# Kernel tuning notes

Hardware: AMD Instinct MI355X
Metric: run time of the kernel (lower is better)

Reference implementation:

```python
import jax, jax.numpy as jnp
import numpy as np

EPS = 1e-5
NEG_INF = -1e30


def layer_norm_seq(x, gamma, beta):
    # Faithful to the custom LayerNorm: normalizes over dim=1 (the T axis of
    # [B, T, C]) with UNBIASED variance (torch.var default), then scales by
    # gamma/beta of shape [C] broadcast over the last axis.
    m = jnp.mean(x, axis=1, keepdims=True)
    v = jnp.var(x, axis=1, keepdims=True, ddof=1)
    return gamma * (x - m) / jnp.sqrt(v + EPS) + beta


def setup_inputs() -> dict:
    key = jax.random.key(0)
    B, T, C, H = 4, 1024, 1024, 16
    hd = C // H  # 64
    ks = jax.random.split(key, 10)
    s_in = 1.0 / np.sqrt(C)
    s_ff = 1.0 / np.sqrt(4 * C)
    return {
        "x": jax.random.normal(ks[0], (B, T, C), dtype=jnp.float32),
        # NOTE: Head uses self.key(x) for BOTH q and k; the query Linear is
        # dead code, so only key/value weights are materialized.
        "Wk": jax.random.uniform(ks[1], (H, C, hd), minval=-s_in, maxval=s_in, dtype=jnp.float32),
        "Wv": jax.random.uniform(ks[2], (H, C, hd), minval=-s_in, maxval=s_in, dtype=jnp.float32),
        "Wp": jax.random.uniform(ks[3], (C, C), minval=-s_in, maxval=s_in, dtype=jnp.float32),
        "bp": jnp.zeros((C,), dtype=jnp.float32),
        "W1": jax.random.uniform(ks[4], (4 * C, C), minval=-s_in, maxval=s_in, dtype=jnp.float32),
        "b1": jnp.zeros((4 * C,), dtype=jnp.float32),
        "W2": jax.random.uniform(ks[5], (C, 4 * C), minval=-s_ff, maxval=s_ff, dtype=jnp.float32),
        "b2": jnp.zeros((C,), dtype=jnp.float32),
        "g1": jnp.ones((C,), dtype=jnp.float32),
        "beta1": jnp.zeros((C,), dtype=jnp.float32),
        "g2": jnp.ones((C,), dtype=jnp.float32),
        "beta2": jnp.zeros((C,), dtype=jnp.float32),
    }


def reference(x, Wk, Wv, Wp, bp, W1, b1, W2, b2, g1, beta1, g2, beta2):
    B, T, C = x.shape
    H, _, hd = Wk.shape
    scale = hd ** -0.5

    # --- self-attention sublayer (pre-LN over sequence axis) ---
    h = layer_norm_seq(x, g1, beta1)
    # q and k BOTH use the key projection (faithful to the original bug).
    qk = jnp.einsum("btc,hcd->bhtd", h, Wk)          # [B,H,T,hd]
    v = jnp.einsum("btc,hcd->bhtd", h, Wv)           # [B,H,T,hd]
    wei = jnp.einsum("bhtd,bhsd->bhts", qk, qk) * scale  # [B,H,T,T]
    causal = jnp.tril(jnp.ones((T, T), dtype=bool))
    wei = jnp.where(causal, wei, NEG_INF)
    wei = jax.nn.softmax(wei, axis=-1)
    attn = jnp.einsum("bhts,bhsd->bthd", wei, v).reshape(B, T, C)
    attn = attn @ Wp.T + bp
    x = x + attn

    # --- feed-forward sublayer ---
    h2 = layer_norm_seq(x, g2, beta2)
    ff = jax.nn.relu(h2 @ W1.T + b1) @ W2.T + b2
    return x + ff
```

## Files before the change

### kernel.cpp

```cpp
#include <hip/hip_runtime.h>
#include <stdint.h>


#define BDIM 256

typedef __attribute__((ext_vector_type(8))) __bf16 bf16x8;
typedef __attribute__((ext_vector_type(4))) float f32x4;

__device__ __forceinline__ unsigned short f2bf(float f) {
    unsigned u = __float_as_uint(f);
    u += 0x7fff + ((u >> 16) & 1);
    return (unsigned short)(u >> 16);
}

__device__ __forceinline__ void gload_lds16(const void* g, void* l) {
    __builtin_amdgcn_global_load_lds(
        (const __attribute__((address_space(1))) void*)g,
        (__attribute__((address_space(3))) void*)l, 16, 0, 0);
}

__global__ void k_cast_bf16(const float* __restrict__ in, unsigned short* __restrict__ out, int n4) {
    int i = blockIdx.x * BDIM + threadIdx.x;
    if (i >= n4) return;
    float4 v = ((const float4*)in)[i];
    ushort4 o;
    o.x = f2bf(v.x); o.y = f2bf(v.y); o.z = f2bf(v.z); o.w = f2bf(v.w);
    ((ushort4*)out)[i] = o;
}

__global__ void k_headT(const float* __restrict__ W, unsigned short* __restrict__ out) {
    __shared__ float tile[64][65];
    const int tid = threadIdx.x;
    const int c0 = blockIdx.x * 64, h = blockIdx.y;
    const float* src = W + ((long)h << 16) + (long)c0 * 64;
    #pragma unroll
    for (int j = 0; j < 16; ++j) {
        int idx = j * 256 + tid;
        tile[idx >> 6][idx & 63] = src[idx];
    }
    __syncthreads();
    #pragma unroll
    for (int j = 0; j < 16; ++j) {
        int idx = j * 256 + tid;
        int d = idx >> 6, c = idx & 63;
        out[(long)(h * 64 + d) * 1024 + c0 + c] = f2bf(tile[c][d]);
    }
}

__global__ void k_ln_part(const float* __restrict__ x, float* __restrict__ psum, float* __restrict__ psq) {
    int c = blockIdx.x * BDIM + threadIdx.x;
    int tc = blockIdx.y, b = blockIdx.z;
    const float* p = x + ((long)b << 20) + ((long)tc * 128) * 1024 + c;
    float s = 0.f, ss = 0.f;
    for (int t = 0; t < 128; ++t) {
        float v = p[t * 1024];
        s += v; ss += v * v;
    }
    int o = (b * 8 + tc) * 1024 + c;
    psum[o] = s; psq[o] = ss;
}

__global__ void k_ln_fin(const float* __restrict__ psum, const float* __restrict__ psq,
                         float* __restrict__ mean, float* __restrict__ rstd) {
    int i = blockIdx.x * BDIM + threadIdx.x;
    int b = i >> 10, c = i & 1023;
    float s = 0.f, ss = 0.f;
    for (int j = 0; j < 8; ++j) {
        s  += psum[(b * 8 + j) * 1024 + c];
        ss += psq[(b * 8 + j) * 1024 + c];
    }
    float m = s * (1.0f / 1024.0f);
    float var = (ss - 1024.0f * m * m) * (1.0f / 1023.0f);
    mean[i] = m;
    rstd[i] = rsqrtf(var + 1e-5f);
}

__global__ void k_ln_apply(const float* __restrict__ x, const float* __restrict__ mean,
                           const float* __restrict__ rstd, const float* __restrict__ g,
                           const float* __restrict__ beta, unsigned short* __restrict__ out) {
    int i = blockIdx.x * BDIM + threadIdx.x;
    int flat = i << 2;
    int b = flat >> 20, c = flat & 1023;
    float4 xv = ((const float4*)x)[i];
    float4 mv = *(const float4*)&mean[(b << 10) + c];
    float4 rv = *(const float4*)&rstd[(b << 10) + c];
    float4 gv = *(const float4*)&g[c];
    float4 bv = *(const float4*)&beta[c];
    ushort4 o;
    o.x = f2bf(gv.x * (xv.x - mv.x) * rv.x + bv.x);
    o.y = f2bf(gv.y * (xv.y - mv.y) * rv.y + bv.y);
    o.z = f2bf(gv.z * (xv.z - mv.z) * rv.z + bv.z);
    o.w = f2bf(gv.w * (xv.w - mv.w) * rv.w + bv.w);
    ((ushort4*)out)[i] = o;
}

__global__ void k_addbias(const float* __restrict__ res, const float* __restrict__ bias,
                          float* __restrict__ out) {
    int i = blockIdx.x * BDIM + threadIdx.x;
    int c = (i << 2) & 1023;
    float4 r = ((const float4*)res)[i];
    float4 bv = *(const float4*)&bias[c];
    r.x += bv.x; r.y += bv.y; r.z += bv.z; r.w += bv.w;
    ((float4*)out)[i] = r;
}

template <int EPI>
__global__ __launch_bounds__(256, 3) void k_gemm_bt(
    const unsigned short* __restrict__ A, const unsigned short* __restrict__ B,
    void* __restrict__ Cv, const float* __restrict__ bias, const float* __restrict__ res,
    int N, int K, int ldA, int ldB, long sA, long sB, long sC)
{
    __shared__ __align__(16) unsigned short As[2][128 * 32];
    __shared__ __align__(16) unsigned short Bs[2][128 * 32];
    const int tid = threadIdx.x;
    const int wave = tid >> 6, lane = tid & 63;
    const long bz = blockIdx.z;
    const int m0 = blockIdx.y * 128, n0 = blockIdx.x * 128;
    const unsigned short* Ab = A + bz * sA;
    const unsigned short* Bb = B + bz * sB;

    const int srow = wave * 16 + (lane >> 2);
    const int skel = (lane & 3) * 8;
    const unsigned short* gA0 = Ab + (long)(m0 + srow) * ldA + skel;
    const unsigned short* gB0 = Bb + (long)(n0 + srow) * ldB + skel;
    const long rowoffA = (long)64 * ldA;
    const long rowoffB = (long)64 * ldB;
    const int lofs = wave * 512;

    f32x4 acc[4][4] = {};

    const int wm = (wave >> 1) * 64, wn = (wave & 1) * 64;
    const int lr = lane & 15, lg = lane >> 4;
    const int aoff = lg * 8;

    gload_lds16(gA0, &As[0][lofs]);
    gload_lds16(gA0 + rowoffA, &As[0][2048 + lofs]);
    gload_lds16(gB0, &Bs[0][lofs]);
    gload_lds16(gB0 + rowoffB, &Bs[0][2048 + lofs]);
    asm volatile("s_waitcnt vmcnt(0)" ::: "memory");
    __builtin_amdgcn_s_barrier();
    __builtin_amdgcn_sched_barrier(0);

    int cur = 0;
    for (int kt = 0; kt < K; kt += 32) {
        const int nxt = cur ^ 1;
        if (kt + 32 < K) {
            gload_lds16(gA0 + kt + 32, &As[nxt][lofs]);
            gload_lds16(gA0 + rowoffA + kt + 32, &As[nxt][2048 + lofs]);
            gload_lds16(gB0 + kt + 32, &Bs[nxt][lofs]);
            gload_lds16(gB0 + rowoffB + kt + 32, &Bs[nxt][2048 + lofs]);
        }
        bf16x8 af[4], bfr[4];
        #pragma unroll
        for (int i = 0; i < 4; ++i) {
            af[i]  = *(const bf16x8*)&As[cur][(wm + i * 16 + lr) * 32 + aoff];
            bfr[i] = *(const bf16x8*)&Bs[cur][(wn + i * 16 + lr) * 32 + aoff];
        }
        #pragma unroll
        for (int i = 0; i < 4; ++i)
            #pragma unroll
            for (int j = 0; j < 4; ++j)
                acc[i][j] = __builtin_amdgcn_mfma_f32_16x16x32_bf16(af[i], bfr[j], acc[i][j], 0, 0, 0);
        asm volatile("s_waitcnt vmcnt(0)" ::: "memory");
        __builtin_amdgcn_s_barrier();
        __builtin_amdgcn_sched_barrier(0);
        cur = nxt;
    }

    const int cr0 = lg * 4;
    #pragma unroll
    for (int mi = 0; mi < 4; ++mi) {
        #pragma unroll
        for (int r = 0; r < 4; ++r) {
            const int row = m0 + wm + mi * 16 + cr0 + r;
            const long rb = bz * sC + (long)row * N;
            #pragma unroll
            for (int nj = 0; nj < 4; ++nj) {
                const int col = n0 + wn + nj * 16 + lr;
                float v = acc[mi][nj][r];
                if (EPI == 0) {
                    ((unsigned short*)Cv)[rb + col] = f2bf(v);
                } else if (EPI == 1) {
                    ((float*)Cv)[rb + col] = v + bias[col] + res[rb + col];
                } else if (EPI == 2) {
                    v += bias[col];
                    ((unsigned short*)Cv)[rb + col] = f2bf(v > 0.f ? v : 0.f);
                } else {
                    atomicAdd(&((float*)Cv)[rb + col], v);
                }
            }
        }
    }
}

#define CEXP 0.18033688f
#define PSTRIDE 72

__global__ __launch_bounds__(256, 2) void k_attn(
    const unsigned short* __restrict__ qk, const unsigned short* __restrict__ vt,
    unsigned short* __restrict__ ctx)
{
    __shared__ __align__(16) unsigned short Ks[64 * 64];
    __shared__ __align__(16) unsigned short Vs[64 * 64];
    __shared__ __align__(16) unsigned short P[4][16 * PSTRIDE];
    const int tid = threadIdx.x;
    const int wave = tid >> 6, lane = tid & 63;
    const int bh = blockIdx.x >> 3, pairIdx = blockIdx.x & 7;
    const int b = bh >> 4, h = bh & 15;
    const int lr = lane & 15, lg = lane >> 4;

    const int swz = (lr & 7) << 4;
    const int cby0 = (lg * 16) ^ swz;
    const int cby1 = (64 + lg * 16) ^ swz;
    const int srow_l = lane >> 3;
    const int scol = ((lane & 7) * 8) ^ (srow_l << 3);

    unsigned short* Pw = P[wave];
    char* KsB = (char*)Ks;
    char* VsB = (char*)Vs;
    const unsigned short* qbase = qk + ((long)b << 20) + h * 64;
    const unsigned short* vb    = vt + ((long)(b * 16 + h) << 16);

    #pragma unroll 1
    for (int phase = 0; phase < 2; ++phase) {
        const int qb = phase ? (15 - pairIdx) : pairIdx;
        const int q0 = qb << 6;
        const int qw = q0 + wave * 16;

        const unsigned short* qrow = qbase + (long)(qw + lr) * 1024 + lg * 8;
        const bf16x8 aq0 = *(const bf16x8*)qrow;
        const bf16x8 aq1 = *(const bf16x8*)(qrow + 32);

        f32x4 acc[4] = {};
        float mrow[4] = {-1e30f, -1e30f, -1e30f, -1e30f};
        float lrow[4] = {0.f, 0.f, 0.f, 0.f};

        for (int c = 0; c <= qb; ++c) {
            const int k0 = c << 6;
            __syncthreads();
            #pragma unroll
            for (int i = 0; i < 2; ++i) {
                const int row = i * 32 + wave * 8 + srow_l;
                gload_lds16(qbase + (long)(k0 + row) * 1024 + scol,
                            KsB + i * 4096 + wave * 1024);
                gload_lds16(vb + (long)row * 1024 + k0 + scol,
                            VsB + i * 4096 + wave * 1024);
            }
            __syncthreads();

            f32x4 s[4];
            #pragma unroll
            for (int t = 0; t < 4; ++t) {
                const int r = t * 16 + lr;
                bf16x8 bk0 = *(const bf16x8*)(KsB + r * 128 + cby0);
                bf16x8 bk1 = *(const bf16x8*)(KsB + r * 128 + cby1);
                f32x4 z = {};
                z = __builtin_amdgcn_mfma_f32_16x16x32_bf16(aq0, bk0, z, 0, 0, 0);
                s[t] = __builtin_amdgcn_mfma_f32_16x16x32_bf16(aq1, bk1, z, 0, 0, 0);
            }
            if (c == qb) {
                #pragma unroll
                for (int t = 0; t < 4; ++t) {
                    const int col = t * 16 + lr;
                    #pragma unroll
                    for (int r = 0; r < 4; ++r)
                        if (col > wave * 16 + lg * 4 + r) s[t][r] = -1e30f;
                }
            }
            float fac[4];
            #pragma unroll
            for (int r = 0; r < 4; ++r) {
                float v = fmaxf(fmaxf(s[0][r], s[1][r]), fmaxf(s[2][r], s[3][r]));
                v = fmaxf(v, __shfl_xor(v, 1));
                v = fmaxf(v, __shfl_xor(v, 2));
                v = fmaxf(v, __shfl_xor(v, 4));
                v = fmaxf(v, __shfl_xor(v, 8));
                float mn = fmaxf(mrow[r], v);
                fac[r] = exp2f((mrow[r] - mn) * CEXP);
                mrow[r] = mn;
            }
            float psum[4] = {0.f, 0.f, 0.f, 0.f};
            #pragma unroll
            for (int t = 0; t < 4; ++t) {
                #pragma unroll
                for (int r = 0; r < 4; ++r) {
                    float p = exp2f((s[t][r] - mrow[r]) * CEXP);
                    psum[r] += p;
                    Pw[(lg * 4 + r) * PSTRIDE + t * 16 + lr] = f2bf(p);
                }
            }
            #pragma unroll
            for (int r = 0; r < 4; ++r) {
                float v = psum[r];
                v += __shfl_xor(v, 1); v += __shfl_xor(v, 2);
                v += __shfl_xor(v, 4); v += __shfl_xor(v, 8);
                lrow[r] = lrow[r] * fac[r] + v;
            }
            #pragma unroll
            for (int ni = 0; ni < 4; ++ni)
                #pragma unroll
                for (int r = 0; r < 4; ++r)
                    acc[ni][r] *= fac[r];
            const bf16x8 pa0 = *(const bf16x8*)&Pw[lr * PSTRIDE + lg * 8];
            const bf16x8 pa1 = *(const bf16x8*)&Pw[lr * PSTRIDE + 32 + lg * 8];
            #pragma unroll
            for (int ni = 0; ni < 4; ++ni) {
                const int vr = ni * 16 + lr;
                bf16x8 bv0 = *(const bf16x8*)(VsB + vr * 128 + cby0);
                bf16x8 bv1 = *(const bf16x8*)(VsB + vr * 128 + cby1);
                acc[ni] = __builtin_amdgcn_mfma_f32_16x16x32_bf16(pa0, bv0, acc[ni], 0, 0, 0);
                acc[ni] = __builtin_amdgcn_mfma_f32_16x16x32_bf16(pa1, bv1, acc[ni], 0, 0, 0);
            }
        }

        unsigned short* crow = ctx + ((long)(b * 1024 + qw)) * 1024 + h * 64;
        #pragma unroll
        for (int r = 0; r < 4; ++r) {
            const float inv = 1.0f / lrow[r];
            #pragma unroll
            for (int ni = 0; ni < 4; ++ni)
                crow[(long)(lg * 4 + r) * 1024 + ni * 16 + lr] = f2bf(acc[ni][r] * inv);
        }
    }
}

extern "C" void kernel_launch(void* const* d_in, const int* in_sizes, int n_in,
                              void* d_out, int out_size, void* d_ws, size_t ws_size,
                              hipStream_t stream)
{
    const float* x   = (const float*)d_in[0];
    const float* Wk  = (const float*)d_in[1];
    const float* Wv  = (const float*)d_in[2];
    const float* Wp  = (const float*)d_in[3];
    const float* bp  = (const float*)d_in[4];
    const float* W1  = (const float*)d_in[5];
    const float* b1  = (const float*)d_in[6];
    const float* W2  = (const float*)d_in[7];
    const float* b2  = (const float*)d_in[8];
    const float* g1  = (const float*)d_in[9];
    const float* be1 = (const float*)d_in[10];
    const float* g2  = (const float*)d_in[11];
    const float* be2 = (const float*)d_in[12];
    float* out = (float*)d_out;

    char* ws = (char*)d_ws;
    const long MB = 1024 * 1024;
    unsigned short* BkT = (unsigned short*)(ws);
    unsigned short* WvT = (unsigned short*)(ws + 2 * MB);
    unsigned short* WpB = (unsigned short*)(ws + 4 * MB);
    unsigned short* W1B = (unsigned short*)(ws + 6 * MB);
    unsigned short* W2B = (unsigned short*)(ws + 14 * MB);
    unsigned short* hB  = (unsigned short*)(ws + 22 * MB);
    unsigned short* qkB = (unsigned short*)(ws + 30 * MB);
    unsigned short* VtB = (unsigned short*)(ws + 38 * MB);
    unsigned short* ctx = (unsigned short*)(ws + 46 * MB);
    unsigned short* ff1 = (unsigned short*)(ws + 30 * MB);
    float* x2   = (float*)(ws + 62 * MB);
    float* psum = (float*)(ws + 78 * MB);
    float* psq  = (float*)(ws + 78 * MB + 128 * 1024);
    float* mean = (float*)(ws + 78 * MB + 256 * 1024);
    float* rstd = (float*)(ws + 78 * MB + 272 * 1024);

    k_cast_bf16<<<1024, BDIM, 0, stream>>>(Wp, WpB, 262144);
    k_cast_bf16<<<4096, BDIM, 0, stream>>>(W1, W1B, 1048576);
    k_cast_bf16<<<4096, BDIM, 0, stream>>>(W2, W2B, 1048576);
    k_headT<<<dim3(16, 16), BDIM, 0, stream>>>(Wk, BkT);
    k_headT<<<dim3(16, 16), BDIM, 0, stream>>>(Wv, WvT);

    k_ln_part<<<dim3(4, 8, 4), BDIM, 0, stream>>>(x, psum, psq);
    k_ln_fin<<<16, BDIM, 0, stream>>>(psum, psq, mean, rstd);
    k_ln_apply<<<4096, BDIM, 0, stream>>>(x, mean, rstd, g1, be1, hB);

    k_gemm_bt<0><<<dim3(8, 32, 1), BDIM, 0, stream>>>(hB, BkT, qkB, nullptr, nullptr, 1024, 1024, 1024, 1024, 0, 0, 0);
    k_gemm_bt<0><<<dim3(8, 8, 4), BDIM, 0, stream>>>(WvT, hB, VtB, nullptr, nullptr, 1024, 1024, 1024, 1024, 0, MB, MB);

    k_attn<<<512, BDIM, 0, stream>>>(qkB, VtB, ctx);

    k_gemm_bt<1><<<dim3(8, 32, 1), BDIM, 0, stream>>>(ctx, WpB, x2, bp, x, 1024, 1024, 1024, 1024, 0, 0, 0);

    k_ln_part<<<dim3(4, 8, 4), BDIM, 0, stream>>>(x2, psum, psq);
    k_ln_fin<<<16, BDIM, 0, stream>>>(psum, psq, mean, rstd);
    k_ln_apply<<<4096, BDIM, 0, stream>>>(x2, mean, rstd, g2, be2, hB);

    k_gemm_bt<2><<<dim3(32, 32, 1), BDIM, 0, stream>>>(hB, W1B, ff1, b1, nullptr, 4096, 1024, 1024, 1024, 0, 0, 0);

    k_addbias<<<4096, BDIM, 0, stream>>>(x2, b2, out);
    k_gemm_bt<3><<<dim3(8, 32, 2), BDIM, 0, stream>>>(ff1, W2B, out, nullptr, nullptr, 1024, 2048, 4096, 4096, 2048, 2048, 0);
}
```

Baseline: 384.1 us.

## Triple-buffer GEMM LDS pipeline with XOR swizzle and deeper split-K for FF2

Moves the bf16 GEMM from a double-buffered to a triple-buffered LDS pipeline. Tiles are prefetched two steps ahead and the loop waits with vmcnt(4), so one in-flight stage overlaps compute and there is only one barrier per iteration. It also XOR-swizzles the k-chunk position per row on both the global-to-LDS writes and the fragment reads, to reduce LDS bank conflicts. The FF2 GEMM's split-K goes from 2 to 4 slices to raise the block count, at the cost of more atomic or partial-sum traffic into the output and 50% more LDS per block, which may lower occupancy.

```diff
diff --git a/kernel.cpp b/kernel.cpp
--- a/kernel.cpp
+++ b/kernel.cpp
@@ -110,45 +110,53 @@
     void* __restrict__ Cv, const float* __restrict__ bias, const float* __restrict__ res,
     int N, int K, int ldA, int ldB, long sA, long sB, long sC)
 {
-    __shared__ __align__(16) unsigned short As[2][128 * 32];
-    __shared__ __align__(16) unsigned short Bs[2][128 * 32];
+    __shared__ __align__(16) unsigned short As[3][128 * 32];
+    __shared__ __align__(16) unsigned short Bs[3][128 * 32];
     const int tid = threadIdx.x;
     const int wave = tid >> 6, lane = tid & 63;
     const long bz = blockIdx.z;
     const int m0 = blockIdx.y * 128, n0 = blockIdx.x * 128;
-    const unsigned short* Ab = A + bz * sA;
-    const unsigned short* Bb = B + bz * sB;
 
     const int srow = wave * 16 + (lane >> 2);
-    const int skel = (lane & 3) * 8;
-    const unsigned short* gA0 = Ab + (long)(m0 + srow) * ldA + skel;
-    const unsigned short* gB0 = Bb + (long)(n0 + srow) * ldB + skel;
+    const int kbs = (lane & 3) ^ ((srow >> 1) & 3);
+    const unsigned short* gA0 = A + bz * sA + (long)(m0 + srow) * ldA + kbs * 8;
+    const unsigned short* gB0 = B + bz * sB + (long)(n0 + srow) * ldB + kbs * 8;
     const long rowoffA = (long)64 * ldA;
     const long rowoffB = (long)64 * ldB;
     const int lofs = wave * 512;
 
     f32x4 acc[4][4] = {};
-
     const int wm = (wave >> 1) * 64, wn = (wave & 1) * 64;
     const int lr = lane & 15, lg = lane >> 4;
-    const int aoff = lg * 8;
-
-    gload_lds16(gA0, &As[0][lofs]);
-    gload_lds16(gA0 + rowoffA, &As[0][2048 + lofs]);
-    gload_lds16(gB0, &Bs[0][lofs]);
-    gload_lds16(gB0 + rowoffB, &Bs[0][2048 + lofs]);
-    asm volatile("s_waitcnt vmcnt(0)" ::: "memory");
-    __builtin_amdgcn_s_barrier();
-    __builtin_amdgcn_sched_barrier(0);
+    const int aoff = (lg ^ ((lr >> 1) & 3)) * 8;
+
+    const int nsteps = K >> 5;
+
+    auto stage = [&](int step, int buf) {
+        const long ko = (long)step * 32;
+        unsigned short* a = &As[buf][lofs];
+        unsigned short* b = &Bs[buf][lofs];
+        gload_lds16(gA0 + ko, a);
+        gload_lds16(gA0 + rowoffA + ko, a + 2048);
+        gload_lds16(gB0 + ko, b);
+        gload_lds16(gB0 + rowoffB + ko, b + 2048);
+    };
+
+    stage(0, 0);
+    stage(1, 1);
 
     int cur = 0;
-    for (int kt = 0; kt < K; kt += 32) {
-        const int nxt = cur ^ 1;
-        if (kt + 32 < K) {
-            gload_lds16(gA0 + kt + 32, &As[nxt][lofs]);
-            gload_lds16(gA0 + rowoffA + kt + 32, &As[nxt][2048 + lofs]);
-            gload_lds16(gB0 + kt + 32, &Bs[nxt][lofs]);
-            gload_lds16(gB0 + rowoffB + kt + 32, &Bs[nxt][2048 + lofs]);
+    for (int t = 0; t < nsteps; ++t) {
+        if (t + 1 < nsteps) {
+            asm volatile("s_waitcnt vmcnt(4)" ::: "memory");
+        } else {
+            asm volatile("s_waitcnt vmcnt(0)" ::: "memory");
+        }
+        __builtin_amdgcn_s_barrier();
+        __builtin_amdgcn_sched_barrier(0);
+        if (t + 2 < nsteps) {
+            int pbuf = cur + 2; if (pbuf >= 3) pbuf -= 3;
+            stage(t + 2, pbuf);
         }
         bf16x8 af[4], bfr[4];
         #pragma unroll
@@ -161,10 +169,8 @@
             #pragma unroll
             for (int j = 0; j < 4; ++j)
                 acc[i][j] = __builtin_amdgcn_mfma_f32_16x16x32_bf16(af[i], bfr[j], acc[i][j], 0, 0, 0);
-        asm volatile("s_waitcnt vmcnt(0)" ::: "memory");
-        __builtin_amdgcn_s_barrier();
         __builtin_amdgcn_sched_barrier(0);
-        cur = nxt;
+        cur = cur + 1; if (cur == 3) cur = 0;
     }
 
     const int cr0 = lg * 4;
@@ -385,5 +391,5 @@
     k_gemm_bt<2><<<dim3(32, 32, 1), BDIM, 0, stream>>>(hB, W1B, ff1, b1, nullptr, 4096, 1024, 1024, 1024, 0, 0, 0);
 
     k_addbias<<<4096, BDIM, 0, stream>>>(x2, b2, out);
-    k_gemm_bt<3><<<dim3(8, 32, 2), BDIM, 0, stream>>>(ff1, W2B, out, nullptr, nullptr, 1024, 2048, 4096, 4096, 2048, 2048, 0);
-}
+    k_gemm_bt<3><<<dim3(8, 32, 4), BDIM, 0, stream>>>(ff1, W2B, out, nullptr, nullptr, 1024, 1024, 4096, 4096, 1024, 1024, 0);
+}
```

Result: slower. 420.3 us (+9.4%).

## Add 256x256 tiled GEMM for FFN and XOR-swizzle LDS layout

Applied to the files above, without the earlier changes.

Adds a new 512-thread GEMM kernel with 256x256 output tiles and a K-step of 64, used for both FFN GEMMs (the second one now split-K over four slices with atomic adds). The LDS tiles in both this kernel and the existing 128x128 GEMM are XOR-swizzled on the k-chunk index to cut LDS bank conflicts on fragment reads. The larger tile raises arithmetic intensity per load and adds setprio around the MFMA bursts. In exchange it uses more registers and LDS per block, launches fewer blocks (256 for FFN1), and the deeper split-K adds more atomic traffic into the output.

```diff
diff --git a/kernel.cpp b/kernel.cpp
--- a/kernel.cpp
+++ b/kernel.cpp
@@ -116,27 +116,28 @@
     const int wave = tid >> 6, lane = tid & 63;
     const long bz = blockIdx.z;
     const int m0 = blockIdx.y * 128, n0 = blockIdx.x * 128;
-    const unsigned short* Ab = A + bz * sA;
-    const unsigned short* Bb = B + bz * sB;
 
     const int srow = wave * 16 + (lane >> 2);
-    const int skel = (lane & 3) * 8;
-    const unsigned short* gA0 = Ab + (long)(m0 + srow) * ldA + skel;
-    const unsigned short* gB0 = Bb + (long)(n0 + srow) * ldB + skel;
+    const int kbs = (lane & 3) ^ ((srow >> 1) & 3);
+    const unsigned short* gA0 = A + bz * sA + (long)(m0 + srow) * ldA + kbs * 8;
+    const unsigned short* gB0 = B + bz * sB + (long)(n0 + srow) * ldB + kbs * 8;
     const long rowoffA = (long)64 * ldA;
     const long rowoffB = (long)64 * ldB;
     const int lofs = wave * 512;
 
     f32x4 acc[4][4] = {};
-
     const int wm = (wave >> 1) * 64, wn = (wave & 1) * 64;
     const int lr = lane & 15, lg = lane >> 4;
-    const int aoff = lg * 8;
-
-    gload_lds16(gA0, &As[0][lofs]);
-    gload_lds16(gA0 + rowoffA, &As[0][2048 + lofs]);
-    gload_lds16(gB0, &Bs[0][lofs]);
-    gload_lds16(gB0 + rowoffB, &Bs[0][2048 + lofs]);
+    const int aoff = (lg ^ ((lr >> 1) & 3)) * 8;
+
+    auto stage = [&](int kt, int buf) {
+        gload_lds16(gA0 + kt, &As[buf][lofs]);
+        gload_lds16(gA0 + rowoffA + kt, &As[buf][2048 + lofs]);
+        gload_lds16(gB0 + kt, &Bs[buf][lofs]);
+        gload_lds16(gB0 + rowoffB + kt, &Bs[buf][2048 + lofs]);
+    };
+
+    stage(0, 0);
     asm volatile("s_waitcnt vmcnt(0)" ::: "memory");
     __builtin_amdgcn_s_barrier();
     __builtin_amdgcn_sched_barrier(0);
@@ -144,12 +145,7 @@
     int cur = 0;
     for (int kt = 0; kt < K; kt += 32) {
         const int nxt = cur ^ 1;
-        if (kt + 32 < K) {
-            gload_lds16(gA0 + kt + 32, &As[nxt][lofs]);
-            gload_lds16(gA0 + rowoffA + kt + 32, &As[nxt][2048 + lofs]);
-            gload_lds16(gB0 + kt + 32, &Bs[nxt][lofs]);
-            gload_lds16(gB0 + rowoffB + kt + 32, &Bs[nxt][2048 + lofs]);
-        }
+        if (kt + 32 < K) stage(kt + 32, nxt);
         bf16x8 af[4], bfr[4];
         #pragma unroll
         for (int i = 0; i < 4; ++i) {
@@ -182,7 +178,102 @@
                     ((unsigned short*)Cv)[rb + col] = f2bf(v);
                 } else if (EPI == 1) {
                     ((float*)Cv)[rb + col] = v + bias[col] + res[rb + col];
-                } else if (EPI == 2) {
+                } else {
+                    v += bias[col];
+                    ((unsigned short*)Cv)[rb + col] = f2bf(v > 0.f ? v : 0.f);
+                }
+            }
+        }
+    }
+}
+
+template <int EPI>
+__global__ __launch_bounds__(512, 2) void k_gemm256(
+    const unsigned short* __restrict__ A, const unsigned short* __restrict__ B,
+    void* __restrict__ Cv, const float* __restrict__ bias,
+    int N, int K, int ldA, int ldB)
+{
+    __shared__ __align__(16) unsigned short As[2][2][128 * 64];
+    __shared__ __align__(16) unsigned short Bs[2][2][128 * 64];
+    const int tid = threadIdx.x;
+    const int wv = tid >> 6, l = tid & 63;
+    const int m0 = blockIdx.y * 256, n0 = blockIdx.x * 256;
+    const long koff = (long)blockIdx.z * K;
+
+    const int lr = l & 15, lg = l >> 4;
+
+    const int srow = wv * 16 + (l >> 3);
+    const int g0 = (l & 7) ^ (l >> 4);
+    const int g1 = (l & 7) ^ (4 + (l >> 4));
+    const unsigned short* pA = A + koff + (long)(m0 + srow) * ldA;
+    const unsigned short* pB = B + koff + (long)(n0 + srow) * ldB;
+    const long l8A = (long)8 * ldA, l128A = (long)128 * ldA;
+    const long l8B = (long)8 * ldB, l128B = (long)128 * ldB;
+    const int dst0 = wv * 1024;
+
+    auto stage = [&](int k0, int d) {
+        #pragma unroll
+        for (int h = 0; h < 2; ++h) {
+            gload_lds16(pA + (long)h * l128A + k0 + g0 * 8, &As[d][h][dst0]);
+            gload_lds16(pA + (long)h * l128A + l8A + k0 + g1 * 8, &As[d][h][dst0 + 512]);
+            gload_lds16(pB + (long)h * l128B + k0 + g0 * 8, &Bs[d][h][dst0]);
+            gload_lds16(pB + (long)h * l128B + l8B + k0 + g1 * 8, &Bs[d][h][dst0 + 512]);
+        }
+    };
+
+    f32x4 acc[8][4] = {};
+    const int wh = wv >> 2;
+    const int bh = (wv & 3) >> 1;
+    const int brow0 = (wv & 1) * 64;
+    const int swz = (lr >> 1) & 7;
+
+    stage(0, 0);
+
+    const int nt = K >> 6;
+    int cur = 0;
+    for (int t = 0; t < nt; ++t) {
+        asm volatile("s_waitcnt vmcnt(0)" ::: "memory");
+        __builtin_amdgcn_s_barrier();
+        __builtin_amdgcn_sched_barrier(0);
+        if (t + 1 < nt) stage((t + 1) << 6, cur ^ 1);
+        const unsigned short* Ah = &As[cur][wh][0];
+        const unsigned short* Bh = &Bs[cur][bh][0];
+        #pragma unroll
+        for (int ks = 0; ks < 2; ++ks) {
+            const int kb = ((ks * 4 + lg) ^ swz) * 8;
+            bf16x8 af[8], bfr[4];
+            #pragma unroll
+            for (int fm = 0; fm < 8; ++fm)
+                af[fm] = *(const bf16x8*)&Ah[(fm * 16 + lr) * 64 + kb];
+            #pragma unroll
+            for (int fn = 0; fn < 4; ++fn)
+                bfr[fn] = *(const bf16x8*)&Bh[(brow0 + fn * 16 + lr) * 64 + kb];
+            asm volatile("s_waitcnt lgkmcnt(0)" ::: "memory");
+            __builtin_amdgcn_sched_barrier(0);
+            __builtin_amdgcn_s_setprio(1);
+            #pragma unroll
+            for (int fm = 0; fm < 8; ++fm)
+                #pragma unroll
+                for (int fn = 0; fn < 4; ++fn)
+                    acc[fm][fn] = __builtin_amdgcn_mfma_f32_16x16x32_bf16(af[fm], bfr[fn], acc[fm][fn], 0, 0, 0);
+            __builtin_amdgcn_s_setprio(0);
+            __builtin_amdgcn_sched_barrier(0);
+        }
+        cur ^= 1;
+    }
+
+    const int wm = (wv >> 2) * 128, wn = (wv & 3) * 64;
+    #pragma unroll
+    for (int fm = 0; fm < 8; ++fm) {
+        #pragma unroll
+        for (int r = 0; r < 4; ++r) {
+            const int row = m0 + wm + fm * 16 + lg * 4 + r;
+            const long rb = (long)row * N;
+            #pragma unroll
+            for (int fn = 0; fn < 4; ++fn) {
+                const int col = n0 + wn + fn * 16 + lr;
+                float v = acc[fm][fn][r];
+                if (EPI == 2) {
                     v += bias[col];
                     ((unsigned short*)Cv)[rb + col] = f2bf(v > 0.f ? v : 0.f);
                 } else {
@@ -382,8 +473,8 @@
     k_ln_fin<<<16, BDIM, 0, stream>>>(psum, psq, mean, rstd);
     k_ln_apply<<<4096, BDIM, 0, stream>>>(x2, mean, rstd, g2, be2, hB);
 
-    k_gemm_bt<2><<<dim3(32, 32, 1), BDIM, 0, stream>>>(hB, W1B, ff1, b1, nullptr, 4096, 1024, 1024, 1024, 0, 0, 0);
+    k_gemm256<2><<<dim3(16, 16, 1), 512, 0, stream>>>(hB, W1B, ff1, b1, 4096, 1024, 1024, 1024);
 
     k_addbias<<<4096, BDIM, 0, stream>>>(x2, b2, out);
-    k_gemm_bt<3><<<dim3(8, 32, 2), BDIM, 0, stream>>>(ff1, W2B, out, nullptr, nullptr, 1024, 2048, 4096, 4096, 2048, 2048, 0);
-}
+    k_gemm256<3><<<dim3(4, 16, 4), 512, 0, stream>>>(ff1, W2B, out, nullptr, 1024, 1024, 4096, 4096);
+}
```

After: 403.0 us. 4.9% more time.

## Deepen GEMM K-tile to 64 with XOR-swizzled LDS and grid remapping

Applied to the files above, without the earlier changes.

The bf16 GEMM now stages 64-wide K tiles instead of 32, which halves the number of barrier/wait iterations. LDS rows are XOR-swizzled so the 128-byte row reads avoid bank conflicts. Workgroup IDs are remapped across groups of 8 to improve L2 locality, and MFMA bursts run at raised wave priority. LDS use doubles to 64KB per block, so occupancy is lowered from 3 to 2 blocks per CU, and K must be a multiple of 64.

```diff
diff --git a/kernel.cpp b/kernel.cpp
--- a/kernel.cpp
+++ b/kernel.cpp
@@ -105,79 +105,87 @@
 }
 
 template <int EPI>
-__global__ __launch_bounds__(256, 3) void k_gemm_bt(
+__global__ __launch_bounds__(256, 2) void k_gemm_bt(
     const unsigned short* __restrict__ A, const unsigned short* __restrict__ B,
     void* __restrict__ Cv, const float* __restrict__ bias, const float* __restrict__ res,
     int N, int K, int ldA, int ldB, long sA, long sB, long sC)
 {
-    __shared__ __align__(16) unsigned short As[2][128 * 32];
-    __shared__ __align__(16) unsigned short Bs[2][128 * 32];
+    __shared__ __align__(16) unsigned short As[2][128 * 64];
+    __shared__ __align__(16) unsigned short Bs[2][128 * 64];
     const int tid = threadIdx.x;
-    const int wave = tid >> 6, lane = tid & 63;
+    const int wv = tid >> 6, l = tid & 63;
     const long bz = blockIdx.z;
-    const int m0 = blockIdx.y * 128, n0 = blockIdx.x * 128;
-    const unsigned short* Ab = A + bz * sA;
-    const unsigned short* Bb = B + bz * sB;
-
-    const int srow = wave * 16 + (lane >> 2);
-    const int skel = (lane & 3) * 8;
-    const unsigned short* gA0 = Ab + (long)(m0 + srow) * ldA + skel;
-    const unsigned short* gB0 = Bb + (long)(n0 + srow) * ldB + skel;
-    const long rowoffA = (long)64 * ldA;
-    const long rowoffB = (long)64 * ldB;
-    const int lofs = wave * 512;
+
+    const int gx = gridDim.x;
+    const int nwg = gx * gridDim.y;
+    int lin = blockIdx.y * gx + blockIdx.x;
+    lin = (lin & 7) * (nwg >> 3) + (lin >> 3);
+    const int m0 = (lin / gx) * 128, n0 = (lin % gx) * 128;
+
+    const int lr = l & 15, lg = l >> 4;
+
+    const int srow = wv * 32 + (l >> 3);
+    const unsigned short* pA = A + bz * sA + (long)(m0 + srow) * ldA;
+    const unsigned short* pB = B + bz * sB + (long)(n0 + srow) * ldB;
+
+    auto stage = [&](int k0, int d) {
+        #pragma unroll
+        for (int L = 0; L < 4; ++L) {
+            const int g = ((l & 7) ^ ((L * 4 + (l >> 4)) & 7)) * 8;
+            gload_lds16(pA + (long)(L * 8) * ldA + k0 + g, &As[d][(wv * 4 + L) * 512]);
+            gload_lds16(pB + (long)(L * 8) * ldB + k0 + g, &Bs[d][(wv * 4 + L) * 512]);
+        }
+    };
 
     f32x4 acc[4][4] = {};
-
-    const int wm = (wave >> 1) * 64, wn = (wave & 1) * 64;
-    const int lr = lane & 15, lg = lane >> 4;
-    const int aoff = lg * 8;
-
-    gload_lds16(gA0, &As[0][lofs]);
-    gload_lds16(gA0 + rowoffA, &As[0][2048 + lofs]);
-    gload_lds16(gB0, &Bs[0][lofs]);
-    gload_lds16(gB0 + rowoffB, &Bs[0][2048 + lofs]);
+    const int wm = (wv >> 1) * 64, wn = (wv & 1) * 64;
+    const int rsw = (lr >> 1) & 7;
+
+    const int nt = K >> 6;
+    stage(0, 0);
     asm volatile("s_waitcnt vmcnt(0)" ::: "memory");
     __builtin_amdgcn_s_barrier();
     __builtin_amdgcn_sched_barrier(0);
 
-    int cur = 0;
-    for (int kt = 0; kt < K; kt += 32) {
-        const int nxt = cur ^ 1;
-        if (kt + 32 < K) {
-            gload_lds16(gA0 + kt + 32, &As[nxt][lofs]);
-            gload_lds16(gA0 + rowoffA + kt + 32, &As[nxt][2048 + lofs]);
-            gload_lds16(gB0 + kt + 32, &Bs[nxt][lofs]);
-            gload_lds16(gB0 + rowoffB + kt + 32, &Bs[nxt][2048 + lofs]);
-        }
-        bf16x8 af[4], bfr[4];
+    for (int t = 0; t < nt; ++t) {
+        const int d = t & 1;
+        if (t + 1 < nt) stage((t + 1) << 6, d ^ 1);
         #pragma unroll
-        for (int i = 0; i < 4; ++i) {
-            af[i]  = *(const bf16x8*)&As[cur][(wm + i * 16 + lr) * 32 + aoff];
-            bfr[i] = *(const bf16x8*)&Bs[cur][(wn + i * 16 + lr) * 32 + aoff];
-        }
-        #pragma unroll
-        for (int i = 0; i < 4; ++i)
-            #pragma unroll
-            for (int j = 0; j < 4; ++j)
-                acc[i][j] = __builtin_amdgcn_mfma_f32_16x16x32_bf16(af[i], bfr[j], acc[i][j], 0, 0, 0);
+        for (int ks = 0; ks < 2; ++ks) {
+            bf16x8 af[4], bfr[4];
+            #pragma unroll
+            for (int fm = 0; fm < 4; ++fm)
+                af[fm] = *(const bf16x8*)&As[d][(wm + fm * 16 + lr) * 64 + (((ks * 4 + lg) ^ rsw) * 8)];
+            #pragma unroll
+            for (int fn = 0; fn < 4; ++fn)
+                bfr[fn] = *(const bf16x8*)&Bs[d][(wn + fn * 16 + lr) * 64 + (((ks * 4 + lg) ^ rsw) * 8)];
+            asm volatile("s_waitcnt lgkmcnt(0)" ::: "memory");
+            __builtin_amdgcn_sched_barrier(0);
+            __builtin_amdgcn_s_setprio(1);
+            #pragma unroll
+            for (int fm = 0; fm < 4; ++fm)
+                #pragma unroll
+                for (int fn = 0; fn < 4; ++fn)
+                    acc[fm][fn] = __builtin_amdgcn_mfma_f32_16x16x32_bf16(af[fm], bfr[fn], acc[fm][fn], 0, 0, 0);
+            __builtin_amdgcn_s_setprio(0);
+            __builtin_amdgcn_sched_barrier(0);
+        }
         asm volatile("s_waitcnt vmcnt(0)" ::: "memory");
         __builtin_amdgcn_s_barrier();
         __builtin_amdgcn_sched_barrier(0);
-        cur = nxt;
     }
 
     const int cr0 = lg * 4;
     #pragma unroll
-    for (int mi = 0; mi < 4; ++mi) {
+    for (int fm = 0; fm < 4; ++fm) {
         #pragma unroll
         for (int r = 0; r < 4; ++r) {
-            const int row = m0 + wm + mi * 16 + cr0 + r;
+            const int row = m0 + wm + fm * 16 + cr0 + r;
             const long rb = bz * sC + (long)row * N;
             #pragma unroll
-            for (int nj = 0; nj < 4; ++nj) {
-                const int col = n0 + wn + nj * 16 + lr;
-                float v = acc[mi][nj][r];
+            for (int fn = 0; fn < 4; ++fn) {
+                const int col = n0 + wn + fn * 16 + lr;
+                float v = acc[fm][fn][r];
                 if (EPI == 0) {
                     ((unsigned short*)Cv)[rb + col] = f2bf(v);
                 } else if (EPI == 1) {
```

Result: faster. 366.1 us (-4.7%).
